# Kernel tuning notes

Hardware: AMD Instinct MI355X
Metric: run time of the kernel (lower is better)

## Reference

```python
import jax, jax.numpy as jnp
import numpy as np

EPS = 1e-5

def _gnn_edge_layer(m, W, b, g, beta, src, dst, n_nodes):
    # DGL send_and_recv(copy_e('m'), sum) : scatter-sum edge feats to dst nodes
    h = jax.ops.segment_sum(m, dst, num_segments=n_nodes)          # [N, d_in]
    # apply_edges: cat(src_h, m) -> Linear -> BatchNorm1d (batch stats) -> relu
    x = jnp.concatenate([h[src], m], axis=1)                        # [E, 2*d_in]
    x = x @ W.T + b                                                 # [E, d_out]
    mu = jnp.mean(x, axis=0)
    var = jnp.var(x, axis=0)                                        # biased, as torch BN training
    x = (x - mu) * jax.lax.rsqrt(var + EPS) * g + beta
    return jax.nn.relu(x), h

def setup_inputs() -> dict:
    key = jax.random.key(0)
    ks = jax.random.split(key, 6)
    E, N = 1_000_000, 100_000
    d0, d1, d2 = 64, 128, 64
    return {
        "m": jax.random.normal(ks[0], (E, d0), jnp.float32),
        "W0": jax.random.normal(ks[1], (d1, 2 * d0), jnp.float32) / np.sqrt(2 * d0),
        "b0": jnp.zeros((d1,), jnp.float32),
        "g0": jnp.ones((d1,), jnp.float32),
        "beta0": jnp.zeros((d1,), jnp.float32),
        "W1": jax.random.normal(ks[2], (d2, 2 * d1), jnp.float32) / np.sqrt(2 * d1),
        "b1": jnp.zeros((d2,), jnp.float32),
        "g1": jnp.ones((d2,), jnp.float32),
        "beta1": jnp.zeros((d2,), jnp.float32),
        "src": jax.random.randint(ks[3], (E,), 0, N, jnp.int32),
        "dst": jax.random.randint(ks[4], (E,), 0, N, jnp.int32),
        "n_nodes": N,
    }

def reference(m, W0, b0, g0, beta0, W1, b1, g1, beta1, src, dst, n_nodes):
    m, h = _gnn_edge_layer(m, W0, b0, g0, beta0, src, dst, n_nodes)
    m, h = _gnn_edge_layer(m, W1, b1, g1, beta1, src, dst, n_nodes)
    # Simple_edge_encoder.forward returns feat_nodes of the last layer
    return h
```

## Files before the change

### kernel.cpp

```cpp
#include <hip/hip_runtime.h>
#include <hip/hip_bf16.h>
#include <stdint.h>


typedef __attribute__((ext_vector_type(8))) short bf16x8;
typedef __attribute__((ext_vector_type(4))) float f32x4;

__device__ inline uint16_t f2bf(float x) {
    uint32_t u = __float_as_uint(x);
    return (uint16_t)((u + 0x7fffu + ((u >> 16) & 1u)) >> 16);
}
__device__ inline float bf2f(uint32_t lo16) { return __uint_as_float(lo16 << 16); }

__global__ __launch_bounds__(256) void k_hist(const int* __restrict__ dst,
                                              int* __restrict__ cnt, int E)
{
    int e = blockIdx.x * 256 + threadIdx.x;
    if (e < E) atomicAdd(&cnt[dst[e]], 1);
}

__global__ __launch_bounds__(256) void k_scanA(const int* __restrict__ cnt,
                                               int* __restrict__ bsum, int N)
{
    int t = threadIdx.x, b = blockIdx.x;
    int i4 = b * 256 + t;
    int4 v = make_int4(0, 0, 0, 0);
    if (i4 < (N >> 2)) v = ((const int4*)cnt)[i4];
    int s = v.x + v.y + v.z + v.w;
    #pragma unroll
    for (int o = 1; o < 64; o <<= 1) s += __shfl_xor(s, o, 64);
    __shared__ int ws[4];
    if ((t & 63) == 0) ws[t >> 6] = s;
    __syncthreads();
    if (t == 0) bsum[b] = ws[0] + ws[1] + ws[2] + ws[3];
}

__global__ __launch_bounds__(128) void k_scanB(int* __restrict__ bsum, int nb)
{
    int t = threadIdx.x;
    int v = (t < nb) ? bsum[t] : 0;
    int lane = t & 63, w = t >> 6;
    int x = v;
    #pragma unroll
    for (int o = 1; o < 64; o <<= 1) {
        int y = __shfl_up(x, o, 64);
        if (lane >= o) x += y;
    }
    __shared__ int wt[2];
    if (lane == 63) wt[w] = x;
    __syncthreads();
    if (w == 1) x += wt[0];
    if (t < nb) bsum[t] = x - v;
}

__global__ __launch_bounds__(256) void k_scanC(const int* __restrict__ cnt,
                                               const int* __restrict__ bsum,
                                               int* __restrict__ off,
                                               int* __restrict__ cur, int N)
{
    int t = threadIdx.x, b = blockIdx.x;
    int i4 = b * 256 + t;
    bool ok = (i4 < (N >> 2));
    int4 v = make_int4(0, 0, 0, 0);
    if (ok) v = ((const int4*)cnt)[i4];
    int s = v.x + v.y + v.z + v.w;
    int lane = t & 63, w = t >> 6;
    int x = s;
    #pragma unroll
    for (int o = 1; o < 64; o <<= 1) {
        int y = __shfl_up(x, o, 64);
        if (lane >= o) x += y;
    }
    __shared__ int wt[4];
    if (lane == 63) wt[w] = x;
    __syncthreads();
    int wbase = 0;
    for (int k = 0; k < w; k++) wbase += wt[k];
    int excl = bsum[b] + wbase + x - s;
    if (ok) {
        int4 o4;
        o4.x = excl; o4.y = excl + v.x; o4.z = o4.y + v.y; o4.w = o4.z + v.z;
        ((int4*)off)[i4] = o4;
        ((int4*)cur)[i4] = o4;
    }
}

__global__ __launch_bounds__(256) void k_perm(const int* __restrict__ dst,
                                              int* __restrict__ cur,
                                              int* __restrict__ perm, int E)
{
    int e = blockIdx.x * 256 + threadIdx.x;
    if (e < E) {
        int pos = atomicAdd(&cur[dst[e]], 1);
        perm[pos] = e;
    }
}

__global__ __launch_bounds__(256) void k1_gather_h1(
    const float* __restrict__ m, const int* __restrict__ perm,
    const int* __restrict__ off, const int* __restrict__ cur,
    const int* __restrict__ src,
    ushort* __restrict__ h1bf, int* __restrict__ srcsort, int N)
{
    const int lane = threadIdx.x & 63;
    const int n = blockIdx.x * 4 + (threadIdx.x >> 6);
    if (n >= N) return;
    const int s0 = off[n], s1 = cur[n];

    for (int j = s0 + lane; j < s1; j += 64) srcsort[j] = src[perm[j]];

    float a0 = 0.f, a1 = 0.f, a2 = 0.f, a3 = 0.f;
    int i = s0;
    for (; i + 4 <= s1; i += 4) {
        int e0 = perm[i], e1 = perm[i + 1], e2 = perm[i + 2], e3 = perm[i + 3];
        a0 += m[(size_t)e0 * 64 + lane];
        a1 += m[(size_t)e1 * 64 + lane];
        a2 += m[(size_t)e2 * 64 + lane];
        a3 += m[(size_t)e3 * 64 + lane];
    }
    for (; i < s1; i++) a0 += m[(size_t)perm[i] * 64 + lane];
    h1bf[(size_t)n * 64 + lane] = f2bf((a0 + a1) + (a2 + a3));
}

template<bool EDGE>
__global__ __launch_bounds__(256) void gemm_mfma(
    const void* __restrict__ Xv,
    const float* __restrict__ W0,
    int wcol,
    const float* __restrict__ bias,
    const float* __restrict__ A,
    const int*   __restrict__ srcS,
    const int*   __restrict__ perm,
    float* __restrict__ outA,
    ushort* __restrict__ xbf,
    float* __restrict__ gstats,
    int R, int ntiles)
{
    const int t  = threadIdx.x;
    const int l  = t & 63;
    const int lm = l & 15;
    const int q  = l >> 4;
    const int wv = t >> 6;

    bf16x8 bfr[8][2];
    #pragma unroll
    for (int nt = 0; nt < 8; nt++)
        #pragma unroll
        for (int ks = 0; ks < 2; ks++) {
            const float* wp = W0 + (nt * 16 + lm) * 128 + wcol + ks * 32 + q * 8;
            bf16x8 bf;
            #pragma unroll
            for (int j = 0; j < 8; j++) ((ushort*)&bf)[j] = f2bf(wp[j]);
            bfr[nt][ks] = bf;
        }
    float bs[8];
    if (!EDGE) {
        #pragma unroll
        for (int nt = 0; nt < 8; nt++) bs[nt] = bias[nt * 16 + lm];
    }

    __shared__ float sst[256];
    float lsum[8], lsq[8];
    if (EDGE) {
        #pragma unroll
        for (int nt = 0; nt < 8; nt++) { lsum[nt] = 0.f; lsq[nt] = 0.f; }
        sst[t] = 0.f;
        __syncthreads();
    }

    for (int tile = blockIdx.x; tile < ntiles; tile += gridDim.x) {
        const int r0 = tile * 64 + wv * 16;

        bf16x8 af[2];
        if (EDGE) {
            const int pr = perm[r0 + lm];
            const float* xp = (const float*)Xv + (size_t)pr * 64 + q * 8;
            #pragma unroll
            for (int ks = 0; ks < 2; ks++) {
                float4 w0 = *(const float4*)(xp + ks * 32);
                float4 w1 = *(const float4*)(xp + ks * 32 + 4);
                bf16x8 bf;
                ((ushort*)&bf)[0] = f2bf(w0.x); ((ushort*)&bf)[1] = f2bf(w0.y);
                ((ushort*)&bf)[2] = f2bf(w0.z); ((ushort*)&bf)[3] = f2bf(w0.w);
                ((ushort*)&bf)[4] = f2bf(w1.x); ((ushort*)&bf)[5] = f2bf(w1.y);
                ((ushort*)&bf)[6] = f2bf(w1.z); ((ushort*)&bf)[7] = f2bf(w1.w);
                af[ks] = bf;
            }
        } else {
            const ushort* xp = (const ushort*)Xv + (size_t)(r0 + lm) * 64 + q * 8;
            af[0] = *(const bf16x8*)xp;
            af[1] = *(const bf16x8*)(xp + 32);
        }

        f32x4 acc[8];
        #pragma unroll
        for (int nt = 0; nt < 8; nt++) acc[nt] = (f32x4){0.f, 0.f, 0.f, 0.f};
        #pragma unroll
        for (int ks = 0; ks < 2; ks++)
            #pragma unroll
            for (int nt = 0; nt < 8; nt++)
                acc[nt] = __builtin_amdgcn_mfma_f32_16x16x32_bf16(
                              af[ks], bfr[nt][ks], acc[nt], 0, 0, 0);

        if (!EDGE) {
            #pragma unroll
            for (int r = 0; r < 4; r++) {
                int row = r0 + q * 4 + r;
                if (row < R) {
                    #pragma unroll
                    for (int nt = 0; nt < 8; nt++)
                        outA[(size_t)row * 128 + nt * 16 + lm] = acc[nt][r] + bs[nt];
                }
            }
        } else {
            int4 rA = *(const int4*)(srcS + r0 + q * 4);
            const int* rAp = &rA.x;
            #pragma unroll
            for (int r = 0; r < 4; r++) {
                int row = r0 + q * 4 + r;
                const float* Ar = A + (size_t)rAp[r] * 128;
                ushort* xo = xbf + (size_t)row * 128 + lm;
                #pragma unroll
                for (int nt = 0; nt < 8; nt++) {
                    float y = acc[nt][r] + Ar[nt * 16 + lm];
                    lsum[nt] += y;
                    lsq[nt]  += y * y;
                    xo[nt * 16] = f2bf(y);
                }
            }
        }
    }

    if (EDGE) {
        #pragma unroll
        for (int nt = 0; nt < 8; nt++) {
            #pragma unroll
            for (int o = 16; o < 64; o <<= 1) {
                lsum[nt] += __shfl_xor(lsum[nt], o, 64);
                lsq[nt]  += __shfl_xor(lsq[nt],  o, 64);
            }
        }
        __syncthreads();
        if (l < 16) {
            #pragma unroll
            for (int nt = 0; nt < 8; nt++) {
                atomicAdd(&sst[nt * 16 + l],       lsum[nt]);
                atomicAdd(&sst[128 + nt * 16 + l], lsq[nt]);
            }
        }
        __syncthreads();
        atomicAdd(&gstats[t], sst[t]);
    }
}

__global__ void k4_finalize(const float* __restrict__ gstats,
                            const float* __restrict__ g0,
                            const float* __restrict__ beta0,
                            float* __restrict__ sc, float Einv)
{
    int j = threadIdx.x;
    float mu  = gstats[j] * Einv;
    float var = gstats[128 + j] * Einv - mu * mu;
    float s   = g0[j] * rsqrtf(var + 1e-5f);
    sc[j]       = s;
    sc[128 + j] = beta0[j] - mu * s;
}

__global__ __launch_bounds__(256) void k5_gather_out(
    const ushort* __restrict__ xbf,
    const int* __restrict__ off, const int* __restrict__ cur,
    const float* __restrict__ sc, float* __restrict__ out, int N)
{
    const int lane = threadIdx.x & 63;
    const int n = blockIdx.x * 4 + (threadIdx.x >> 6);
    if (n >= N) return;
    float2 s = ((const float2*)sc)[lane];
    float2 b = ((const float2*)(sc + 128))[lane];
    const int s0 = off[n], s1 = cur[n];
    float a0 = 0.f, a1 = 0.f, b0 = 0.f, b1 = 0.f;
    float c0 = 0.f, c1 = 0.f, d0 = 0.f, d1 = 0.f;
    int i = s0;
    for (; i + 4 <= s1; i += 4) {
        uint32_t p0 = *(const uint32_t*)(xbf + (size_t)i * 128 + 2 * lane);
        uint32_t p1 = *(const uint32_t*)(xbf + (size_t)(i + 1) * 128 + 2 * lane);
        uint32_t p2 = *(const uint32_t*)(xbf + (size_t)(i + 2) * 128 + 2 * lane);
        uint32_t p3 = *(const uint32_t*)(xbf + (size_t)(i + 3) * 128 + 2 * lane);
        a0 += fmaxf(bf2f(p0 & 0xffffu) * s.x + b.x, 0.f);
        a1 += fmaxf(bf2f(p0 >> 16)     * s.y + b.y, 0.f);
        b0 += fmaxf(bf2f(p1 & 0xffffu) * s.x + b.x, 0.f);
        b1 += fmaxf(bf2f(p1 >> 16)     * s.y + b.y, 0.f);
        c0 += fmaxf(bf2f(p2 & 0xffffu) * s.x + b.x, 0.f);
        c1 += fmaxf(bf2f(p2 >> 16)     * s.y + b.y, 0.f);
        d0 += fmaxf(bf2f(p3 & 0xffffu) * s.x + b.x, 0.f);
        d1 += fmaxf(bf2f(p3 >> 16)     * s.y + b.y, 0.f);
    }
    for (; i < s1; i++) {
        uint32_t p = *(const uint32_t*)(xbf + (size_t)i * 128 + 2 * lane);
        a0 += fmaxf(bf2f(p & 0xffffu) * s.x + b.x, 0.f);
        a1 += fmaxf(bf2f(p >> 16)     * s.y + b.y, 0.f);
    }
    ((float2*)(out + (size_t)n * 128))[lane] =
        make_float2((a0 + b0) + (c0 + d0), (a1 + b1) + (c1 + d1));
}

extern "C" void kernel_launch(void* const* d_in, const int* in_sizes, int n_in,
                              void* d_out, int out_size, void* d_ws, size_t ws_size,
                              hipStream_t stream)
{
    const float* m     = (const float*)d_in[0];
    const float* W0    = (const float*)d_in[1];
    const float* b0    = (const float*)d_in[2];
    const float* g0    = (const float*)d_in[3];
    const float* beta0 = (const float*)d_in[4];
    const int*   src   = (const int*)d_in[9];
    const int*   dst   = (const int*)d_in[10];
    float* out = (float*)d_out;

    const int E = in_sizes[0] / 64;
    const int N = out_size / 128;
    const int ntA = (N + 63) / 64;
    const int Npad = ntA * 64;
    const int ntE = E / 64;
    const int nb  = (N + 1023) / 1024;

    auto align = [](size_t x) { return (x + 255) & ~(size_t)255; };
    char* ws = (char*)d_ws;
    size_t o_h1  = 0;
    size_t o_A   = align(o_h1 + (size_t)Npad * 64 * 2);
    size_t o_x   = align(o_A  + (size_t)N * 128 * 4);
    size_t o_gs  = align(o_x  + (size_t)E * 128 * 2);
    size_t o_sc  = align(o_gs + 256 * 4);
    size_t o_cnt = align(o_sc + 256 * 4);
    size_t o_off = align(o_cnt + (size_t)N * 4);
    size_t o_cur = align(o_off + (size_t)N * 4);
    size_t o_pm  = align(o_cur + (size_t)N * 4);
    size_t o_bs  = align(o_pm  + (size_t)E * 4);
    size_t o_ss  = align(o_bs  + 1024 * 4);
    ushort*   h1bf = (ushort*)(ws + o_h1);
    float*    A    = (float*)(ws + o_A);
    ushort*   xbf  = (ushort*)(ws + o_x);
    float*    gs   = (float*)(ws + o_gs);
    float*    sc   = (float*)(ws + o_sc);
    int*      cnt  = (int*)(ws + o_cnt);
    int*      off  = (int*)(ws + o_off);
    int*      cur  = (int*)(ws + o_cur);
    int*      perm = (int*)(ws + o_pm);
    int*      bsum = (int*)(ws + o_bs);
    int*      srcs = (int*)(ws + o_ss);

    hipMemsetAsync(cnt, 0, (size_t)N * 4, stream);
    hipMemsetAsync(gs, 0, 256 * 4, stream);

    k_hist<<<(E + 255) / 256, 256, 0, stream>>>(dst, cnt, E);
    k_scanA<<<nb, 256, 0, stream>>>(cnt, bsum, N);
    k_scanB<<<1, 128, 0, stream>>>(bsum, nb);
    k_scanC<<<nb, 256, 0, stream>>>(cnt, bsum, off, cur, N);
    k_perm<<<(E + 255) / 256, 256, 0, stream>>>(dst, cur, perm, E);

    k1_gather_h1<<<(N + 3) / 4, 256, 0, stream>>>(m, perm, off, cur, src,
                                                  h1bf, srcs, N);

    gemm_mfma<false><<<ntA, 256, 0, stream>>>(h1bf, W0, 0, b0, nullptr, nullptr,
                                              nullptr, A, nullptr, nullptr, N, ntA);

    gemm_mfma<true><<<2048, 256, 0, stream>>>(m, W0, 64, nullptr, A, srcs, perm,
                                              nullptr, xbf, gs, E, ntE);

    k4_finalize<<<1, 128, 0, stream>>>(gs, g0, beta0, sc, 1.0f / (float)E);

    k5_gather_out<<<(N + 3) / 4, 256, 0, stream>>>(xbf, off, cur, sc, out, N);
}
```

Before: 824.1 us.

## Scatter edge features into dst-sorted bf16 buffer once, read contiguously downstream

Adds a scatter kernel that writes each edge's features, converted to bf16, into dst-sorted order once. The node gather and the edge GEMM then read contiguous sorted bf16 rows instead of making random fp32 gathers through the permutation. k_perm now writes the sorted src indices directly, which removes the srcsort pass from the gather kernel. The cost is an extra 128 MB bf16 buffer and one scatter pass, and h1 now sums bf16-rounded inputs, which slightly lowers accuracy.

```diff
diff --git a/kernel.cpp b/kernel.cpp
--- a/kernel.cpp
+++ b/kernel.cpp
@@ -86,51 +86,63 @@
 }
 
 __global__ __launch_bounds__(256) void k_perm(const int* __restrict__ dst,
+                                              const int* __restrict__ src,
                                               int* __restrict__ cur,
-                                              int* __restrict__ perm, int E)
+                                              int* __restrict__ ipos,
+                                              int* __restrict__ srcS, int E)
 {
     int e = blockIdx.x * 256 + threadIdx.x;
     if (e < E) {
         int pos = atomicAdd(&cur[dst[e]], 1);
-        perm[pos] = e;
-    }
+        ipos[e] = pos;
+        srcS[pos] = src[e];
+    }
+}
+
+__global__ __launch_bounds__(256) void k_scatter(const float* __restrict__ m,
+                                                 const int* __restrict__ ipos,
+                                                 ushort* __restrict__ msort, int E)
+{
+    int t = threadIdx.x;
+    int e = blockIdx.x * 16 + (t >> 4);
+    int l16 = t & 15;
+    if (e >= E) return;
+    int p = ipos[e];
+    float4 v = *(const float4*)(m + (size_t)e * 64 + l16 * 4);
+    ushort4 b;
+    b.x = f2bf(v.x); b.y = f2bf(v.y); b.z = f2bf(v.z); b.w = f2bf(v.w);
+    *(ushort4*)(msort + (size_t)p * 64 + l16 * 4) = b;
 }
 
 __global__ __launch_bounds__(256) void k1_gather_h1(
-    const float* __restrict__ m, const int* __restrict__ perm,
+    const ushort* __restrict__ msort,
     const int* __restrict__ off, const int* __restrict__ cur,
-    const int* __restrict__ src,
-    ushort* __restrict__ h1bf, int* __restrict__ srcsort, int N)
+    ushort* __restrict__ h1bf, int N)
 {
     const int lane = threadIdx.x & 63;
     const int n = blockIdx.x * 4 + (threadIdx.x >> 6);
     if (n >= N) return;
     const int s0 = off[n], s1 = cur[n];
-
-    for (int j = s0 + lane; j < s1; j += 64) srcsort[j] = src[perm[j]];
-
     float a0 = 0.f, a1 = 0.f, a2 = 0.f, a3 = 0.f;
     int i = s0;
     for (; i + 4 <= s1; i += 4) {
-        int e0 = perm[i], e1 = perm[i + 1], e2 = perm[i + 2], e3 = perm[i + 3];
-        a0 += m[(size_t)e0 * 64 + lane];
-        a1 += m[(size_t)e1 * 64 + lane];
-        a2 += m[(size_t)e2 * 64 + lane];
-        a3 += m[(size_t)e3 * 64 + lane];
-    }
-    for (; i < s1; i++) a0 += m[(size_t)perm[i] * 64 + lane];
+        a0 += bf2f(msort[(size_t)i * 64 + lane]);
+        a1 += bf2f(msort[(size_t)(i + 1) * 64 + lane]);
+        a2 += bf2f(msort[(size_t)(i + 2) * 64 + lane]);
+        a3 += bf2f(msort[(size_t)(i + 3) * 64 + lane]);
+    }
+    for (; i < s1; i++) a0 += bf2f(msort[(size_t)i * 64 + lane]);
     h1bf[(size_t)n * 64 + lane] = f2bf((a0 + a1) + (a2 + a3));
 }
 
 template<bool EDGE>
 __global__ __launch_bounds__(256) void gemm_mfma(
-    const void* __restrict__ Xv,
+    const ushort* __restrict__ Xv,
     const float* __restrict__ W0,
     int wcol,
     const float* __restrict__ bias,
     const float* __restrict__ A,
     const int*   __restrict__ srcS,
-    const int*   __restrict__ perm,
     float* __restrict__ outA,
     ushort* __restrict__ xbf,
     float* __restrict__ gstats,
@@ -171,36 +183,21 @@
     for (int tile = blockIdx.x; tile < ntiles; tile += gridDim.x) {
         const int r0 = tile * 64 + wv * 16;
 
-        bf16x8 af[2];
-        if (EDGE) {
-            const int pr = perm[r0 + lm];
-            const float* xp = (const float*)Xv + (size_t)pr * 64 + q * 8;
-            #pragma unroll
-            for (int ks = 0; ks < 2; ks++) {
-                float4 w0 = *(const float4*)(xp + ks * 32);
-                float4 w1 = *(const float4*)(xp + ks * 32 + 4);
-                bf16x8 bf;
-                ((ushort*)&bf)[0] = f2bf(w0.x); ((ushort*)&bf)[1] = f2bf(w0.y);
-                ((ushort*)&bf)[2] = f2bf(w0.z); ((ushort*)&bf)[3] = f2bf(w0.w);
-                ((ushort*)&bf)[4] = f2bf(w1.x); ((ushort*)&bf)[5] = f2bf(w1.y);
-                ((ushort*)&bf)[6] = f2bf(w1.z); ((ushort*)&bf)[7] = f2bf(w1.w);
-                af[ks] = bf;
-            }
-        } else {
-            const ushort* xp = (const ushort*)Xv + (size_t)(r0 + lm) * 64 + q * 8;
-            af[0] = *(const bf16x8*)xp;
-            af[1] = *(const bf16x8*)(xp + 32);
-        }
+        const ushort* xp = Xv + (size_t)(r0 + lm) * 64 + q * 8;
+        bf16x8 af0 = *(const bf16x8*)xp;
+        bf16x8 af1 = *(const bf16x8*)(xp + 32);
 
         f32x4 acc[8];
         #pragma unroll
         for (int nt = 0; nt < 8; nt++) acc[nt] = (f32x4){0.f, 0.f, 0.f, 0.f};
         #pragma unroll
-        for (int ks = 0; ks < 2; ks++)
-            #pragma unroll
-            for (int nt = 0; nt < 8; nt++)
-                acc[nt] = __builtin_amdgcn_mfma_f32_16x16x32_bf16(
-                              af[ks], bfr[nt][ks], acc[nt], 0, 0, 0);
+        for (int nt = 0; nt < 8; nt++)
+            acc[nt] = __builtin_amdgcn_mfma_f32_16x16x32_bf16(
+                          af0, bfr[nt][0], acc[nt], 0, 0, 0);
+        #pragma unroll
+        for (int nt = 0; nt < 8; nt++)
+            acc[nt] = __builtin_amdgcn_mfma_f32_16x16x32_bf16(
+                          af1, bfr[nt][1], acc[nt], 0, 0, 0);
 
         if (!EDGE) {
             #pragma unroll
@@ -333,20 +330,22 @@
     size_t o_cnt = align(o_sc + 256 * 4);
     size_t o_off = align(o_cnt + (size_t)N * 4);
     size_t o_cur = align(o_off + (size_t)N * 4);
-    size_t o_pm  = align(o_cur + (size_t)N * 4);
-    size_t o_bs  = align(o_pm  + (size_t)E * 4);
+    size_t o_ip  = align(o_cur + (size_t)N * 4);
+    size_t o_bs  = align(o_ip  + (size_t)E * 4);
     size_t o_ss  = align(o_bs  + 1024 * 4);
-    ushort*   h1bf = (ushort*)(ws + o_h1);
-    float*    A    = (float*)(ws + o_A);
-    ushort*   xbf  = (ushort*)(ws + o_x);
-    float*    gs   = (float*)(ws + o_gs);
-    float*    sc   = (float*)(ws + o_sc);
-    int*      cnt  = (int*)(ws + o_cnt);
-    int*      off  = (int*)(ws + o_off);
-    int*      cur  = (int*)(ws + o_cur);
-    int*      perm = (int*)(ws + o_pm);
-    int*      bsum = (int*)(ws + o_bs);
-    int*      srcs = (int*)(ws + o_ss);
+    size_t o_ms  = align(o_ss  + (size_t)E * 4);
+    ushort*   h1bf  = (ushort*)(ws + o_h1);
+    float*    A     = (float*)(ws + o_A);
+    ushort*   xbf   = (ushort*)(ws + o_x);
+    float*    gs    = (float*)(ws + o_gs);
+    float*    sc    = (float*)(ws + o_sc);
+    int*      cnt   = (int*)(ws + o_cnt);
+    int*      off   = (int*)(ws + o_off);
+    int*      cur   = (int*)(ws + o_cur);
+    int*      ipos  = (int*)(ws + o_ip);
+    int*      bsum  = (int*)(ws + o_bs);
+    int*      srcs  = (int*)(ws + o_ss);
+    ushort*   msort = (ushort*)(ws + o_ms);
 
     hipMemsetAsync(cnt, 0, (size_t)N * 4, stream);
     hipMemsetAsync(gs, 0, 256 * 4, stream);
@@ -355,15 +354,16 @@
     k_scanA<<<nb, 256, 0, stream>>>(cnt, bsum, N);
     k_scanB<<<1, 128, 0, stream>>>(bsum, nb);
     k_scanC<<<nb, 256, 0, stream>>>(cnt, bsum, off, cur, N);
-    k_perm<<<(E + 255) / 256, 256, 0, stream>>>(dst, cur, perm, E);
-
-    k1_gather_h1<<<(N + 3) / 4, 256, 0, stream>>>(m, perm, off, cur, src,
-                                                  h1bf, srcs, N);
+    k_perm<<<(E + 255) / 256, 256, 0, stream>>>(dst, src, cur, ipos, srcs, E);
+
+    k_scatter<<<(E + 15) / 16, 256, 0, stream>>>(m, ipos, msort, E);
+
+    k1_gather_h1<<<(N + 3) / 4, 256, 0, stream>>>(msort, off, cur, h1bf, N);
 
     gemm_mfma<false><<<ntA, 256, 0, stream>>>(h1bf, W0, 0, b0, nullptr, nullptr,
-                                              nullptr, A, nullptr, nullptr, N, ntA);
-
-    gemm_mfma<true><<<2048, 256, 0, stream>>>(m, W0, 64, nullptr, A, srcs, perm,
+                                              A, nullptr, nullptr, N, ntA);
+
+    gemm_mfma<true><<<2048, 256, 0, stream>>>(msort, W0, 64, nullptr, A, srcs,
                                               nullptr, xbf, gs, E, ntE);
 
     k4_finalize<<<1, 128, 0, stream>>>(gs, g0, beta0, sc, 1.0f / (float)E);
```

Measured after the change: 797.9 us. 3.2% less time.
